# Optimization experiments

Measured on AMD Instinct MI355X. Metric: run time of the kernel, lower is better.

The kernel has to match this reference:

```python
import jax, jax.numpy as jnp
import numpy as np

B, H, L, D = 8, 4, 1024, 64

def setup_inputs() -> dict:
    key = jax.random.key(0)
    ks = jax.random.split(key, 6)
    s = 1.0 / np.sqrt(D)
    return {
        "X": jax.random.normal(ks[0], (B, H, L, D), dtype=jnp.float32),
        "Y": jax.random.normal(ks[1], (B, H, L, D), dtype=jnp.float32),
        "W1": jax.random.normal(ks[2], (D, D), dtype=jnp.float32) * s,
        "b1": jax.random.normal(ks[3], (D,), dtype=jnp.float32) * s,
        "w2": jax.random.normal(ks[4], (D,), dtype=jnp.float32) * s,
        "b2": jax.random.normal(ks[5], (), dtype=jnp.float32) * s,
    }

def reference(X, Y, W1, b1, w2, b2):
    # Original: net[b,i,j,d] = (lin1(X))[b,d,i]*(lin1(Y))[b,d,j]; out = relu(net @ w2 + b2)
    # Algebraically: out[b,i,j] = relu(sum_d w2[d]*Xf[b,i,d]*Yf[b,j,d] + b2)
    Bx, Hx, Lx, Dx = X.shape
    Xf = X.reshape(-1, Lx, Dx) @ W1.T + b1   # [B*H, L, D]
    Yf = Y.reshape(-1, Lx, Dx) @ W1.T + b1   # [B*H, L, D]
    scores = jnp.einsum('bid,bjd->bij', Xf * w2, Yf) + b2  # [B*H, L, L]
    out = jax.nn.relu(scores)
    return out.reshape(Bx, -1, Lx, Lx)
```

## Files before the change

### kernel.cpp

```cpp
#include <hip/hip_runtime.h>

#define BH 32
#define L  1024
#define D  64

typedef short  short8  __attribute__((ext_vector_type(8)));
typedef __bf16 bf16x8  __attribute__((ext_vector_type(8)));
typedef float  f32x16  __attribute__((ext_vector_type(16)));

__device__ __forceinline__ unsigned short f2bf(float f) {
    union { float f; unsigned u; } v; v.f = f;
    unsigned r = v.u + 0x7fffu + ((v.u >> 16) & 1u);
    return (unsigned short)(r >> 16);
}

__global__ __launch_bounds__(256, 4) void proj_kernel(
    const float* __restrict__ X, const float* __restrict__ Y,
    const float* __restrict__ W1, const float* __restrict__ b1,
    const float* __restrict__ w2,
    unsigned short* __restrict__ Xs, unsigned short* __restrict__ Yf)
{
    __shared__ unsigned short Wl[64 * 72];
    __shared__ unsigned short Al[128 * 72];

    const int tid = threadIdx.x;
    const bool isX = (blockIdx.y == 0);
    const float* src = isX ? X : Y;
    unsigned short* dst = isX ? Xs : Yf;
    const int r0 = blockIdx.x * 128;

    {
        const int d  = tid >> 2;
        const int kb = (tid & 3) * 16;
        const float4* wp = (const float4*)(W1 + d * 64 + kb);
        #pragma unroll
        for (int q = 0; q < 4; ++q) {
            float4 v = wp[q];
            unsigned short* o = &Wl[d * 72 + kb + q * 4];
            o[0] = f2bf(v.x); o[1] = f2bf(v.y); o[2] = f2bf(v.z); o[3] = f2bf(v.w);
        }
    }
    {
        const float4* xp = (const float4*)(src + (size_t)r0 * 64);
        #pragma unroll
        for (int p = 0; p < 8; ++p) {
            int c = tid + 256 * p;
            float4 v = xp[c];
            int row = c >> 4;
            int c4  = (c & 15) * 4;
            unsigned short* o = &Al[row * 72 + c4];
            o[0] = f2bf(v.x); o[1] = f2bf(v.y); o[2] = f2bf(v.z); o[3] = f2bf(v.w);
        }
    }
    __syncthreads();

    const int w   = tid >> 6;
    const int l   = tid & 63;
    const int l31 = l & 31;
    const int lh  = l >> 5;

    f32x16 acc[2] = {};

    const int arow = w * 32 + l31;
    #pragma unroll
    for (int kk = 0; kk < 4; ++kk) {
        int k0 = kk * 16 + lh * 8;
        bf16x8 a = *(const bf16x8*)&Al[arow * 72 + k0];
        #pragma unroll
        for (int nt = 0; nt < 2; ++nt) {
            bf16x8 b = *(const bf16x8*)&Wl[(nt * 32 + l31) * 72 + k0];
            acc[nt] = __builtin_amdgcn_mfma_f32_32x32x16_bf16(a, b, acc[nt], 0, 0, 0);
        }
    }

    #pragma unroll
    for (int nt = 0; nt < 2; ++nt) {
        int d = nt * 32 + l31;
        float bb = b1[d];
        float ww = isX ? w2[d] : 1.0f;
        #pragma unroll
        for (int r = 0; r < 16; ++r) {
            int row = w * 32 + 4 * lh + (r & 3) + 8 * (r >> 2);
            float v = (acc[nt][r] + bb) * ww;
            dst[(size_t)(r0 + row) * 64 + d] = f2bf(v);
        }
    }
}

__global__ __launch_bounds__(256, 4) void score_kernel(
    const unsigned short* __restrict__ Xs, const unsigned short* __restrict__ Yf,
    const float* __restrict__ b2p, float* __restrict__ out)
{
    __shared__ unsigned short As[128 * 72];
    __shared__ unsigned short Bs[128 * 72];

    const int tid = threadIdx.x;
    const int bh  = blockIdx.z;
    const int i0  = blockIdx.y * 128;
    const int j0  = blockIdx.x * 128;

    const unsigned short* aSrc = Xs + ((size_t)bh * L + i0) * D;
    const unsigned short* bSrc = Yf + ((size_t)bh * L + j0) * D;

    #pragma unroll
    for (int p = 0; p < 4; ++p) {
        int c   = tid + 256 * p;
        int row = c >> 3;
        int col = c & 7;
        short8 va = *(const short8*)(aSrc + (size_t)c * 8);
        short8 vb = *(const short8*)(bSrc + (size_t)c * 8);
        *(short8*)&As[row * 72 + col * 8] = va;
        *(short8*)&Bs[row * 72 + col * 8] = vb;
    }
    __syncthreads();

    const int w    = tid >> 6;
    const int l    = tid & 63;
    const int l31  = l & 31;
    const int lh   = l >> 5;
    const int wrow = (w >> 1) * 64;
    const int wcol = (w & 1) * 64;

    f32x16 acc[2][2] = {};

    #pragma unroll
    for (int kk = 0; kk < 4; ++kk) {
        int k0 = kk * 16 + lh * 8;
        bf16x8 a0 = *(const bf16x8*)&As[(wrow +      l31) * 72 + k0];
        bf16x8 a1 = *(const bf16x8*)&As[(wrow + 32 + l31) * 72 + k0];
        bf16x8 b0 = *(const bf16x8*)&Bs[(wcol +      l31) * 72 + k0];
        bf16x8 b1 = *(const bf16x8*)&Bs[(wcol + 32 + l31) * 72 + k0];
        acc[0][0] = __builtin_amdgcn_mfma_f32_32x32x16_bf16(a0, b0, acc[0][0], 0, 0, 0);
        acc[0][1] = __builtin_amdgcn_mfma_f32_32x32x16_bf16(a0, b1, acc[0][1], 0, 0, 0);
        acc[1][0] = __builtin_amdgcn_mfma_f32_32x32x16_bf16(a1, b0, acc[1][0], 0, 0, 0);
        acc[1][1] = __builtin_amdgcn_mfma_f32_32x32x16_bf16(a1, b1, acc[1][1], 0, 0, 0);
    }

    const float b2 = b2p[0];
    float* obase = out + (size_t)bh * L * L;

    #pragma unroll
    for (int ti = 0; ti < 2; ++ti) {
        #pragma unroll
        for (int tj = 0; tj < 2; ++tj) {
            int gj = j0 + wcol + tj * 32 + l31;
            #pragma unroll
            for (int r = 0; r < 16; ++r) {
                int gi = i0 + wrow + ti * 32 + 4 * lh + (r & 3) + 8 * (r >> 2);
                float v = acc[ti][tj][r] + b2;
                v = v > 0.0f ? v : 0.0f;
                obase[(size_t)gi * L + gj] = v;
            }
        }
    }
}

extern "C" void kernel_launch(void* const* d_in, const int* in_sizes, int n_in,
                              void* d_out, int out_size, void* d_ws, size_t ws_size,
                              hipStream_t stream) {
    (void)in_sizes; (void)n_in; (void)out_size; (void)ws_size;
    const float* X  = (const float*)d_in[0];
    const float* Y  = (const float*)d_in[1];
    const float* W1 = (const float*)d_in[2];
    const float* b1 = (const float*)d_in[3];
    const float* w2 = (const float*)d_in[4];
    const float* b2 = (const float*)d_in[5];
    float* out = (float*)d_out;

    unsigned short* Xs = (unsigned short*)d_ws;
    unsigned short* Yf = Xs + (size_t)BH * L * D;

    dim3 pgrid(256, 2, 1);
    proj_kernel<<<pgrid, 256, 0, stream>>>(X, Y, W1, b1, w2, Xs, Yf);

    dim3 ggrid(8, 8, BH);
    score_kernel<<<ggrid, 256, 0, stream>>>(Xs, Yf, b2, out);
}
```

Before: 161.3 us.

## Fuse projection into score kernel, recomputing per-tile projections in shared memory

Merges the projection kernel and the score kernel into one launch. Each block converts its fp32 X and Y tiles to bf16, projects them with W1 in LDS via MFMA, then computes the score tile. This removes the intermediate workspace round trip and a kernel launch. In exchange it recomputes each projection once per opposite tile, reads fp32 inputs redundantly, and lowers the occupancy target.

```diff
diff --git a/kernel.cpp b/kernel.cpp
--- a/kernel.cpp
+++ b/kernel.cpp
@@ -14,20 +14,25 @@
     return (unsigned short)(r >> 16);
 }
 
-__global__ __launch_bounds__(256, 4) void proj_kernel(
+__global__ __launch_bounds__(256, 3) void fused_attnnet_kernel(
     const float* __restrict__ X, const float* __restrict__ Y,
     const float* __restrict__ W1, const float* __restrict__ b1,
-    const float* __restrict__ w2,
-    unsigned short* __restrict__ Xs, unsigned short* __restrict__ Yf)
+    const float* __restrict__ w2, const float* __restrict__ b2p,
+    float* __restrict__ out)
 {
     __shared__ unsigned short Wl[64 * 72];
-    __shared__ unsigned short Al[128 * 72];
+    __shared__ unsigned short As[128 * 72];
+    __shared__ unsigned short Bs[128 * 72];
 
     const int tid = threadIdx.x;
-    const bool isX = (blockIdx.y == 0);
-    const float* src = isX ? X : Y;
-    unsigned short* dst = isX ? Xs : Yf;
-    const int r0 = blockIdx.x * 128;
+    const int bh  = blockIdx.z;
+    const int i0  = blockIdx.y * 128;
+    const int j0  = blockIdx.x * 128;
+
+    const int w   = tid >> 6;
+    const int l   = tid & 63;
+    const int l31 = l & 31;
+    const int lh  = l >> 5;
 
     {
         const int d  = tid >> 2;
@@ -39,101 +44,105 @@
             unsigned short* o = &Wl[d * 72 + kb + q * 4];
             o[0] = f2bf(v.x); o[1] = f2bf(v.y); o[2] = f2bf(v.z); o[3] = f2bf(v.w);
         }
+        const float4* yp = (const float4*)(Y + ((size_t)bh * L + j0) * 64);
+        #pragma unroll
+        for (int p = 0; p < 8; ++p) {
+            int c = tid + 256 * p;
+            float4 v = yp[c];
+            int row = c >> 4;
+            int c4  = (c & 15) * 4;
+            unsigned short* o = &As[row * 72 + c4];
+            o[0] = f2bf(v.x); o[1] = f2bf(v.y); o[2] = f2bf(v.z); o[3] = f2bf(v.w);
+        }
     }
+    __syncthreads();
+
+    f32x16 accY[2] = {};
     {
-        const float4* xp = (const float4*)(src + (size_t)r0 * 64);
+        const int arow = w * 32 + l31;
+        #pragma unroll
+        for (int kk = 0; kk < 4; ++kk) {
+            int k0 = kk * 16 + lh * 8;
+            bf16x8 a = *(const bf16x8*)&As[arow * 72 + k0];
+            #pragma unroll
+            for (int nt = 0; nt < 2; ++nt) {
+                bf16x8 b = *(const bf16x8*)&Wl[(nt * 32 + l31) * 72 + k0];
+                accY[nt] = __builtin_amdgcn_mfma_f32_32x32x16_bf16(a, b, accY[nt], 0, 0, 0);
+            }
+        }
+    }
+    __syncthreads();
+
+    {
+        #pragma unroll
+        for (int nt = 0; nt < 2; ++nt) {
+            int d = nt * 32 + l31;
+            float bb = b1[d];
+            #pragma unroll
+            for (int r = 0; r < 16; ++r) {
+                int row = w * 32 + 4 * lh + (r & 3) + 8 * (r >> 2);
+                Bs[row * 72 + d] = f2bf(accY[nt][r] + bb);
+            }
+        }
+        const float4* xp = (const float4*)(X + ((size_t)bh * L + i0) * 64);
         #pragma unroll
         for (int p = 0; p < 8; ++p) {
             int c = tid + 256 * p;
             float4 v = xp[c];
             int row = c >> 4;
             int c4  = (c & 15) * 4;
-            unsigned short* o = &Al[row * 72 + c4];
+            unsigned short* o = &As[row * 72 + c4];
             o[0] = f2bf(v.x); o[1] = f2bf(v.y); o[2] = f2bf(v.z); o[3] = f2bf(v.w);
         }
     }
     __syncthreads();
 
-    const int w   = tid >> 6;
-    const int l   = tid & 63;
-    const int l31 = l & 31;
-    const int lh  = l >> 5;
-
-    f32x16 acc[2] = {};
-
-    const int arow = w * 32 + l31;
-    #pragma unroll
-    for (int kk = 0; kk < 4; ++kk) {
-        int k0 = kk * 16 + lh * 8;
-        bf16x8 a = *(const bf16x8*)&Al[arow * 72 + k0];
+    f32x16 accX[2] = {};
+    {
+        const int arow = w * 32 + l31;
         #pragma unroll
-        for (int nt = 0; nt < 2; ++nt) {
-            bf16x8 b = *(const bf16x8*)&Wl[(nt * 32 + l31) * 72 + k0];
-            acc[nt] = __builtin_amdgcn_mfma_f32_32x32x16_bf16(a, b, acc[nt], 0, 0, 0);
+        for (int kk = 0; kk < 4; ++kk) {
+            int k0 = kk * 16 + lh * 8;
+            bf16x8 a = *(const bf16x8*)&As[arow * 72 + k0];
+            #pragma unroll
+            for (int nt = 0; nt < 2; ++nt) {
+                bf16x8 b = *(const bf16x8*)&Wl[(nt * 32 + l31) * 72 + k0];
+                accX[nt] = __builtin_amdgcn_mfma_f32_32x32x16_bf16(a, b, accX[nt], 0, 0, 0);
+            }
         }
-    }
-
-    #pragma unroll
-    for (int nt = 0; nt < 2; ++nt) {
-        int d = nt * 32 + l31;
-        float bb = b1[d];
-        float ww = isX ? w2[d] : 1.0f;
-        #pragma unroll
-        for (int r = 0; r < 16; ++r) {
-            int row = w * 32 + 4 * lh + (r & 3) + 8 * (r >> 2);
-            float v = (acc[nt][r] + bb) * ww;
-            dst[(size_t)(r0 + row) * 64 + d] = f2bf(v);
-        }
-    }
-}
-
-__global__ __launch_bounds__(256, 4) void score_kernel(
-    const unsigned short* __restrict__ Xs, const unsigned short* __restrict__ Yf,
-    const float* __restrict__ b2p, float* __restrict__ out)
-{
-    __shared__ unsigned short As[128 * 72];
-    __shared__ unsigned short Bs[128 * 72];
-
-    const int tid = threadIdx.x;
-    const int bh  = blockIdx.z;
-    const int i0  = blockIdx.y * 128;
-    const int j0  = blockIdx.x * 128;
-
-    const unsigned short* aSrc = Xs + ((size_t)bh * L + i0) * D;
-    const unsigned short* bSrc = Yf + ((size_t)bh * L + j0) * D;
-
-    #pragma unroll
-    for (int p = 0; p < 4; ++p) {
-        int c   = tid + 256 * p;
-        int row = c >> 3;
-        int col = c & 7;
-        short8 va = *(const short8*)(aSrc + (size_t)c * 8);
-        short8 vb = *(const short8*)(bSrc + (size_t)c * 8);
-        *(short8*)&As[row * 72 + col * 8] = va;
-        *(short8*)&Bs[row * 72 + col * 8] = vb;
     }
     __syncthreads();
 
-    const int w    = tid >> 6;
-    const int l    = tid & 63;
-    const int l31  = l & 31;
-    const int lh   = l >> 5;
+    {
+        #pragma unroll
+        for (int nt = 0; nt < 2; ++nt) {
+            int d = nt * 32 + l31;
+            float bb = b1[d];
+            float ww = w2[d];
+            #pragma unroll
+            for (int r = 0; r < 16; ++r) {
+                int row = w * 32 + 4 * lh + (r & 3) + 8 * (r >> 2);
+                As[row * 72 + d] = f2bf((accX[nt][r] + bb) * ww);
+            }
+        }
+    }
+    __syncthreads();
+
     const int wrow = (w >> 1) * 64;
     const int wcol = (w & 1) * 64;
 
     f32x16 acc[2][2] = {};
-
     #pragma unroll
     for (int kk = 0; kk < 4; ++kk) {
         int k0 = kk * 16 + lh * 8;
         bf16x8 a0 = *(const bf16x8*)&As[(wrow +      l31) * 72 + k0];
         bf16x8 a1 = *(const bf16x8*)&As[(wrow + 32 + l31) * 72 + k0];
         bf16x8 b0 = *(const bf16x8*)&Bs[(wcol +      l31) * 72 + k0];
-        bf16x8 b1 = *(const bf16x8*)&Bs[(wcol + 32 + l31) * 72 + k0];
-        acc[0][0] = __builtin_amdgcn_mfma_f32_32x32x16_bf16(a0, b0, acc[0][0], 0, 0, 0);
-        acc[0][1] = __builtin_amdgcn_mfma_f32_32x32x16_bf16(a0, b1, acc[0][1], 0, 0, 0);
-        acc[1][0] = __builtin_amdgcn_mfma_f32_32x32x16_bf16(a1, b0, acc[1][0], 0, 0, 0);
-        acc[1][1] = __builtin_amdgcn_mfma_f32_32x32x16_bf16(a1, b1, acc[1][1], 0, 0, 0);
+        bf16x8 b1v = *(const bf16x8*)&Bs[(wcol + 32 + l31) * 72 + k0];
+        acc[0][0] = __builtin_amdgcn_mfma_f32_32x32x16_bf16(a0, b0,  acc[0][0], 0, 0, 0);
+        acc[0][1] = __builtin_amdgcn_mfma_f32_32x32x16_bf16(a0, b1v, acc[0][1], 0, 0, 0);
+        acc[1][0] = __builtin_amdgcn_mfma_f32_32x32x16_bf16(a1, b0,  acc[1][0], 0, 0, 0);
+        acc[1][1] = __builtin_amdgcn_mfma_f32_32x32x16_bf16(a1, b1v, acc[1][1], 0, 0, 0);
     }
 
     const float b2 = b2p[0];
@@ -158,7 +167,7 @@
 extern "C" void kernel_launch(void* const* d_in, const int* in_sizes, int n_in,
                               void* d_out, int out_size, void* d_ws, size_t ws_size,
                               hipStream_t stream) {
-    (void)in_sizes; (void)n_in; (void)out_size; (void)ws_size;
+    (void)in_sizes; (void)n_in; (void)out_size; (void)d_ws; (void)ws_size;
     const float* X  = (const float*)d_in[0];
     const float* Y  = (const float*)d_in[1];
     const float* W1 = (const float*)d_in[2];
@@ -167,12 +176,6 @@
     const float* b2 = (const float*)d_in[5];
     float* out = (float*)d_out;
 
-    unsigned short* Xs = (unsigned short*)d_ws;
-    unsigned short* Yf = Xs + (size_t)BH * L * D;
-
-    dim3 pgrid(256, 2, 1);
-    proj_kernel<<<pgrid, 256, 0, stream>>>(X, Y, W1, b1, w2, Xs, Yf);
-
-    dim3 ggrid(8, 8, BH);
-    score_kernel<<<ggrid, 256, 0, stream>>>(Xs, Yf, b2, out);
+    dim3 grid(8, 8, BH);
+    fused_attnnet_kernel<<<grid, 256, 0, stream>>>(X, Y, W1, b1, w2, b2, out);
 }
```

New measurement: 168.6 us. 4.5% more time.
